# Kernel tuning notes

Measured on AMD Instinct MI355X. Metric: run time of the kernel, lower is better.

Reference implementation:

```python
import jax, jax.numpy as jnp
import numpy as np

H = 128          # hidden_size
EF = 2           # expansion_factor
E = H * EF       # expanded hidden size
K = 4            # conv kernel size
R = 8            # dt_rank = ceil(128/16)
L = 2            # num_layers
BATCH = 2
SEQ = 1024
EPS = 1e-5


def rmsnorm(x, w):
    return x * jax.lax.rsqrt(jnp.mean(x * x, axis=-1, keepdims=True) + EPS) * w


def causal_conv1d(x, w, b):
    # x: (b, l, E); w: (E, 1, K) depthwise; left-pad K-1 => causal, output len l
    xt = jnp.transpose(x, (0, 2, 1))  # (b, E, l)
    out = jax.lax.conv_general_dilated(
        xt, w, window_strides=(1,), padding=[(K - 1, 0)],
        dimension_numbers=("NCH", "OIH", "NCH"), feature_group_count=E)
    out = out + b[None, :, None]
    return jnp.transpose(out, (0, 2, 1))


def sscan(xc, delta, A, Bm, Cm, Dp):
    # xc, delta: (b,l,E); A: (E,n); Bm, Cm: (b,l,n); Dp: (E,)
    deltaA = jnp.exp(jnp.einsum('bld,dn->bldn', delta, A))          # (b,l,E,n)
    deltaBx = jnp.einsum('bld,bln,bld->bldn', delta, Bm, xc)        # (b,l,E,n)

    def step(h, inp):
        dA_t, dBx_t, C_t = inp           # (b,E,n), (b,E,n), (b,n)
        h = dA_t * h + dBx_t
        y = jnp.einsum('bdn,bn->bd', h, C_t)
        return h, y

    b = xc.shape[0]
    h0 = jnp.zeros((b, E, A.shape[1]), dtype=xc.dtype)
    _, ys = jax.lax.scan(
        step, h0,
        (jnp.transpose(deltaA, (1, 0, 2, 3)),
         jnp.transpose(deltaBx, (1, 0, 2, 3)),
         jnp.transpose(Cm, (1, 0, 2))))
    y = jnp.transpose(ys, (1, 0, 2))     # (b,l,E)
    return y + Dp * xc


def mamba_block(x, in_w, in_b, out_w, out_b, pl_w, pl_b, dt_w, dt_b,
                conv_w, conv_b, A_log, Dp):
    xz = x @ in_w + in_b                 # (b,l,2E)
    xc, skip = jnp.split(xz, [E], axis=-1)
    xc = jax.nn.silu(causal_conv1d(xc, conv_w, conv_b))
    # ssm
    A = -jnp.exp(A_log)                  # (E,H)
    dbc = xc @ pl_w + pl_b               # (b,l,R+2H)
    delta, Bm, Cm = jnp.split(dbc, [R, R + H], axis=-1)
    delta = jax.nn.softplus(delta @ dt_w + dt_b)   # (b,l,E)
    y = sscan(xc, delta, A, Bm, Cm, Dp)
    y = y * jax.nn.silu(skip)
    return y @ out_w + out_b


def forward(x, in_w, in_b, out_w, out_b, pl_w, pl_b, dt_w, dt_b,
            conv_w, conv_b, A_log, Dp, norm_w, final_norm_w):
    for i in range(L):
        x = mamba_block(rmsnorm(x, norm_w[i]), in_w[i], in_b[i], out_w[i],
                        out_b[i], pl_w[i], pl_b[i], dt_w[i], dt_b[i],
                        conv_w[i], conv_b[i], A_log[i], Dp[i]) + x
    return rmsnorm(x, final_norm_w)


def setup_inputs() -> dict:
    key = jax.random.key(0)
    ks = jax.random.split(key, 12)
    s = 0.02
    x = jax.random.normal(ks[0], (BATCH, SEQ, H), dtype=jnp.float32)
    in_w = jax.random.normal(ks[1], (L, H, 2 * E)) * s
    in_b = jnp.zeros((L, 2 * E))
    out_w = jax.random.normal(ks[2], (L, E, H)) * s
    out_b = jnp.zeros((L, H))
    pl_w = jax.random.normal(ks[3], (L, E, R + 2 * H)) * s
    pl_b = jnp.zeros((L, R + 2 * H))
    dt_w = jax.random.normal(ks[4], (L, R, E)) * s
    dt_b = jnp.zeros((L, E))
    conv_w = jax.random.normal(ks[5], (L, E, 1, K)) * (1.0 / np.sqrt(K))
    conv_b = jnp.zeros((L, E))
    A_log = jnp.broadcast_to(jnp.log(jnp.arange(1, H + 1, dtype=jnp.float32)),
                             (L, E, H))
    Dp = jnp.ones((L, E))
    norm_w = jnp.ones((L, H))
    final_norm_w = jnp.ones((H,))
    return {"x": x, "in_w": in_w, "in_b": in_b, "out_w": out_w,
            "out_b": out_b, "pl_w": pl_w, "pl_b": pl_b, "dt_w": dt_w,
            "dt_b": dt_b, "conv_w": conv_w, "conv_b": conv_b,
            "A_log": A_log, "Dp": Dp, "norm_w": norm_w,
            "final_norm_w": final_norm_w}


def reference(x, in_w, in_b, out_w, out_b, pl_w, pl_b, dt_w, dt_b,
              conv_w, conv_b, A_log, Dp, norm_w, final_norm_w):
    return forward(x, in_w, in_b, out_w, out_b, pl_w, pl_b, dt_w, dt_b,
                   conv_w, conv_b, A_log, Dp, norm_w, final_norm_w)
```

## Files before the change

kernel.cpp:

```cpp
#include <hip/hip_runtime.h>
#include <hip/hip_bf16.h>

#define HH 128
#define EE 256
#define KK 4
#define RR 8
#define LL 2
#define BB 2
#define SS 1024
#define BT (BB*SS)
#define NJ (RR+2*HH)
#define GG 16
#define CH (SS/GG)
#define EPS 1e-5f
#define LOG2E 1.44269504088896f

__device__ __forceinline__ float silu_f(float v) {
    return v / (1.0f + __expf(-v));
}

__global__ __launch_bounds__(256) void k_wdt(
    const float* __restrict__ plw, const float* __restrict__ plb,
    const float* __restrict__ dtw, const float* __restrict__ dtb,
    float* __restrict__ Wdt, float* __restrict__ bdt)
{
    const int l = blockIdx.x >> 2, q = blockIdx.x & 3;
    const int j = threadIdx.x;
    const float* dtwl = dtw + (size_t)l * RR * EE;
    const float* plwl = plw + (size_t)l * EE * NJ;
    float wr[RR];
    #pragma unroll
    for (int r = 0; r < RR; r++) wr[r] = dtwl[r * EE + j];
    float* Wl = Wdt + (size_t)l * EE * EE;
    for (int e = q * 64; e < q * 64 + 64; e++) {
        float a = 0.0f;
        #pragma unroll
        for (int r = 0; r < RR; r++) a += plwl[(size_t)e * NJ + r] * wr[r];
        Wl[(size_t)e * EE + j] = a;
    }
    if (q == 0) {
        float a = dtb[l * EE + j];
        #pragma unroll
        for (int r = 0; r < RR; r++) a += plb[l * NJ + r] * wr[r];
        bdt[l * EE + j] = a;
    }
}

__global__ __launch_bounds__(512) void k_norm_inproj(
    const float* __restrict__ xin, const float* __restrict__ inw,
    const float* __restrict__ inb, const float* __restrict__ nw,
    float* __restrict__ xz)
{
    __shared__ float xn[8][128];
    const int bt0 = blockIdx.x * 8;
    const int tid = threadIdx.x;
    {
        const int t = tid >> 6, lane = tid & 63;
        const float2 xv = *(const float2*)(xin + (size_t)(bt0 + t) * HH + lane * 2);
        float ss = xv.x*xv.x + xv.y*xv.y;
        #pragma unroll
        for (int m = 32; m >= 1; m >>= 1) ss += __shfl_xor(ss, m);
        const float rs = rsqrtf(ss * (1.0f / HH) + EPS);
        const float2 wv = *(const float2*)(nw + lane * 2);
        xn[t][lane*2+0] = xv.x * rs * wv.x;
        xn[t][lane*2+1] = xv.y * rs * wv.y;
    }
    __syncthreads();
    const int j = tid;
    float acc[8];
    const float bj = inb[j];
    #pragma unroll
    for (int t = 0; t < 8; t++) acc[t] = bj;
    float w0n = inw[0*512 + j], w1n = inw[1*512 + j];
    float w2n = inw[2*512 + j], w3n = inw[3*512 + j];
    for (int k4 = 0; k4 < 32; k4++) {
        const float w0 = w0n, w1 = w1n, w2 = w2n, w3 = w3n;
        if (k4 < 31) {
            const int k = (k4 + 1) * 4;
            w0n = inw[(k+0)*512 + j]; w1n = inw[(k+1)*512 + j];
            w2n = inw[(k+2)*512 + j]; w3n = inw[(k+3)*512 + j];
        }
        const int k = k4 * 4;
        #pragma unroll
        for (int t = 0; t < 8; t++) {
            const float4 xv = *(const float4*)(&xn[t][k]);
            acc[t] += w0*xv.x + w1*xv.y + w2*xv.z + w3*xv.w;
        }
    }
    #pragma unroll
    for (int t = 0; t < 8; t++) xz[(size_t)(bt0 + t) * 512 + j] = acc[t];
}

__global__ __launch_bounds__(512) void k_cbd(
    const float* __restrict__ xz, const float* __restrict__ cw,
    const float* __restrict__ cb, const float* __restrict__ plw,
    const float* __restrict__ plb, const float* __restrict__ Wdt,
    const float* __restrict__ bdt,
    float* __restrict__ xcT, float* __restrict__ BC4,
    float* __restrict__ deltaT, float* __restrict__ sT)
{
    __shared__ float xcb[8][256];
    const int bt0 = blockIdx.x * 8;
    const int tid = threadIdx.x;
    {
        const int e = tid & 255, hf = tid >> 8;
        const int ts = bt0 + hf * 4;
        const float w0 = cw[e*4+0], w1 = cw[e*4+1], w2 = cw[e*4+2], w3 = cw[e*4+3];
        const float bias = cb[e];
        const float* xp = xz + (size_t)ts * 512 + e;
        const bool first = ((ts & (SS-1)) == 0);
        float xm3 = first ? 0.0f : xp[-3*512];
        float xm2 = first ? 0.0f : xp[-2*512];
        float xm1 = first ? 0.0f : xp[-1*512];
        float xcv[4];
        #pragma unroll
        for (int i = 0; i < 4; i++) {
            const float x0 = xp[i*512];
            const float v = bias + w3*x0 + w2*xm1 + w1*xm2 + w0*xm3;
            const float o = silu_f(v);
            xcv[i] = o;
            xcb[hf*4 + i][e] = o;
            xm3 = xm2; xm2 = xm1; xm1 = x0;
        }
        *(float4*)(xcT + (size_t)e * BT + ts) =
            make_float4(xcv[0], xcv[1], xcv[2], xcv[3]);
    }
    __syncthreads();
    const int j = tid & 255, path = tid >> 8;
    if (path == 0) {
        const int nn = j & 127, isC = j >> 7;
        const float* wp = plw + RR + isC * HH + nn;
        float acc[8];
        const float bj = plb[RR + isC * HH + nn];
        #pragma unroll
        for (int t = 0; t < 8; t++) acc[t] = bj;
        float w0n = wp[0*NJ], w1n = wp[1*NJ], w2n = wp[2*NJ], w3n = wp[3*NJ];
        for (int e4 = 0; e4 < 64; e4++) {
            const float w0 = w0n, w1 = w1n, w2 = w2n, w3 = w3n;
            if (e4 < 63) {
                const int e = (e4 + 1) * 4;
                w0n = wp[(size_t)(e+0)*NJ]; w1n = wp[(size_t)(e+1)*NJ];
                w2n = wp[(size_t)(e+2)*NJ]; w3n = wp[(size_t)(e+3)*NJ];
            }
            const int e = e4 * 4;
            #pragma unroll
            for (int t = 0; t < 8; t++) {
                const float4 xv = *(const float4*)(&xcb[t][e]);
                acc[t] += w0*xv.x + w1*xv.y + w2*xv.z + w3*xv.w;
            }
        }
        const int tq0 = bt0 >> 2;
        float* p0 = BC4 + ((size_t)tq0 * 128 + nn) * 8 + isC * 4;
        *(float4*)p0 = make_float4(acc[0], acc[1], acc[2], acc[3]);
        float* p1 = BC4 + ((size_t)(tq0 + 1) * 128 + nn) * 8 + isC * 4;
        *(float4*)p1 = make_float4(acc[4], acc[5], acc[6], acc[7]);
    } else {
        const float* wp = Wdt + j;
        float acc[8];
        const float bj = bdt[j];
        #pragma unroll
        for (int t = 0; t < 8; t++) acc[t] = bj;
        float w0n = wp[0*EE], w1n = wp[1*EE], w2n = wp[2*EE], w3n = wp[3*EE];
        for (int e4 = 0; e4 < 64; e4++) {
            const float w0 = w0n, w1 = w1n, w2 = w2n, w3 = w3n;
            if (e4 < 63) {
                const int e = (e4 + 1) * 4;
                w0n = wp[(size_t)(e+0)*EE]; w1n = wp[(size_t)(e+1)*EE];
                w2n = wp[(size_t)(e+2)*EE]; w3n = wp[(size_t)(e+3)*EE];
            }
            const int e = e4 * 4;
            #pragma unroll
            for (int t = 0; t < 8; t++) {
                const float4 xv = *(const float4*)(&xcb[t][e]);
                acc[t] += w0*xv.x + w1*xv.y + w2*xv.z + w3*xv.w;
            }
        }
        float spv[8], sv[8];
        #pragma unroll
        for (int t = 0; t < 8; t++) {
            const float d = acc[t];
            const float sp = (d > 15.0f) ? d : log1pf(__expf(d));
            spv[t] = sp;
            sv[t] = sp * xcb[t][j];
        }
        float* drp = deltaT + (size_t)j * BT + bt0;
        *(float4*)(drp)     = make_float4(spv[0], spv[1], spv[2], spv[3]);
        *(float4*)(drp + 4) = make_float4(spv[4], spv[5], spv[6], spv[7]);
        float* srp = sT + (size_t)j * BT + bt0;
        *(float4*)(srp)     = make_float4(sv[0], sv[1], sv[2], sv[3]);
        *(float4*)(srp + 4) = make_float4(sv[4], sv[5], sv[6], sv[7]);
    }
}

__global__ __launch_bounds__(128, 4) void k_scan_local(
    const float* __restrict__ BC4, const float* __restrict__ deltaT,
    const float* __restrict__ sT, const float* __restrict__ Alog,
    float* __restrict__ yT, float* __restrict__ hchain,
    float* __restrict__ dsum)
{
    __shared__ float part[2][16][68];
    __shared__ float ybuf[2][CH];
    const int blk = blockIdx.x;
    const int wgid = (blk & 7) * 512 + (blk >> 3);
    const int eq = wgid & 127;
    const int r0 = wgid >> 7;
    const int b = r0 >> 4;
    const int g = r0 & 15;
    const int e0 = eq * 2;
    const int n = threadIdx.x;
    const int t0 = g * CH;

    float An0 = -__expf(Alog[(e0+0) * HH + n]) * LOG2E;
    float An1 = -__expf(Alog[(e0+1) * HH + n]) * LOG2E;
    float h0 = 0.0f, h1 = 0.0f, cum0 = 0.0f, cum1 = 0.0f;
    const float* bc = BC4 + ((size_t)((b * 256 + g * 16) * 128 + n)) * 8;
    const float* dr0 = deltaT + (size_t)(e0+0) * BT + b * SS + t0;
    const float* dr1 = deltaT + (size_t)(e0+1) * BT + b * SS + t0;
    const float* sr0 = sT + (size_t)(e0+0) * BT + b * SS + t0;
    const float* sr1 = sT + (size_t)(e0+1) * BT + b * SS + t0;

    float4 pB = *(const float4*)(bc);
    float4 pC = *(const float4*)(bc + 4);
    float4 pd0 = *(const float4*)dr0, pd1 = *(const float4*)dr1;
    float4 ps0 = *(const float4*)sr0, ps1 = *(const float4*)sr1;

    const int tl = n >> 3, jj = n & 7;
    for (int sc = 0; sc < 4; sc++) {
        #pragma unroll
        for (int q = 0; q < 4; q++) {
            const int qq = sc * 4 + q;
            const float4 cB = pB, cC = pC;
            const float4 cd0 = pd0, cd1 = pd1, cs0 = ps0, cs1 = ps1;
            if (qq < 15) {
                const size_t off = (size_t)(qq + 1) * 1024;
                pB = *(const float4*)(bc + off);
                pC = *(const float4*)(bc + off + 4);
                const int t = (qq + 1) * 4;
                pd0 = *(const float4*)(dr0 + t); pd1 = *(const float4*)(dr1 + t);
                ps0 = *(const float4*)(sr0 + t); ps1 = *(const float4*)(sr1 + t);
            }
            float a;
            a = exp2f(cd0.x*An0); h0 = a*h0 + cs0.x*cB.x; part[0][q*4+0][n] = h0*cC.x;
            a = exp2f(cd0.y*An0); h0 = a*h0 + cs0.y*cB.y; part[0][q*4+1][n] = h0*cC.y;
            a = exp2f(cd0.z*An0); h0 = a*h0 + cs0.z*cB.z; part[0][q*4+2][n] = h0*cC.z;
            a = exp2f(cd0.w*An0); h0 = a*h0 + cs0.w*cB.w; part[0][q*4+3][n] = h0*cC.w;
            a = exp2f(cd1.x*An1); h1 = a*h1 + cs1.x*cB.x; part[1][q*4+0][n] = h1*cC.x;
            a = exp2f(cd1.y*An1); h1 = a*h1 + cs1.y*cB.y; part[1][q*4+1][n] = h1*cC.y;
            a = exp2f(cd1.z*An1); h1 = a*h1 + cs1.z*cB.z; part[1][q*4+2][n] = h1*cC.z;
            a = exp2f(cd1.w*An1); h1 = a*h1 + cs1.w*cB.w; part[1][q*4+3][n] = h1*cC.w;
            cum0 += (cd0.x + cd0.y) + (cd0.z + cd0.w);
            cum1 += (cd1.x + cd1.y) + (cd1.z + cd1.w);
        }
        __syncthreads();
        #pragma unroll
        for (int ee = 0; ee < 2; ee++) {
            float s0 = 0, s1 = 0, s2 = 0, s3 = 0;
            #pragma unroll
            for (int i = 0; i < 4; i++) {
                const float4 p = *(const float4*)(&part[ee][tl][jj*16 + i*4]);
                s0 += p.x; s1 += p.y; s2 += p.z; s3 += p.w;
            }
            float r = (s0 + s1) + (s2 + s3);
            r += __shfl_xor(r, 1); r += __shfl_xor(r, 2); r += __shfl_xor(r, 4);
            if (jj == 0) ybuf[ee][sc*16 + tl] = r;
        }
        __syncthreads();
    }
    {
        const int ee = n >> 6, tt = n & 63;
        yT[(size_t)(e0 + ee) * BT + b * SS + t0 + tt] = ybuf[ee][tt];
    }
    hchain[(size_t)(((b * EE + e0 + 0) * GG) + g) * 128 + n] = h0;
    hchain[(size_t)(((b * EE + e0 + 1) * GG) + g) * 128 + n] = h1;
    if (n == 0) {
        dsum[(b * EE + e0 + 0) * GG + g] = cum0;
        dsum[(b * EE + e0 + 1) * GG + g] = cum1;
    }
}

__global__ __launch_bounds__(128, 4) void k_scan_fix(
    const float* __restrict__ BC4, const float* __restrict__ deltaT,
    const float* __restrict__ Alog, const float* __restrict__ hchain,
    const float* __restrict__ dsum, float* __restrict__ yT)
{
    __shared__ float part[2][16][68];
    __shared__ float ybuf[2][CH];
    const int blk = blockIdx.x;
    const int wgid = (blk & 7) * 480 + (blk >> 3);
    const int eq = wgid & 127;
    const int r0 = wgid >> 7;
    const int b = r0 / 15;
    const int g = 1 + (r0 % 15);
    const int e0 = eq * 2;
    const int n = threadIdx.x;
    const int t0 = g * CH;

    const float An0 = -__expf(Alog[(e0+0) * HH + n]) * LOG2E;
    const float An1 = -__expf(Alog[(e0+1) * HH + n]) * LOG2E;
    float w0 = 0.0f, w1 = 0.0f;
    {
        const size_t hb0 = (size_t)((b * EE + e0 + 0) * GG) * 128 + n;
        const size_t hb1 = (size_t)((b * EE + e0 + 1) * GG) * 128 + n;
        const int db0 = (b * EE + e0 + 0) * GG;
        const int db1 = (b * EE + e0 + 1) * GG;
        for (int gp = 0; gp < g; gp++) {
            const float he0 = hchain[hb0 + (size_t)gp * 128];
            const float he1 = hchain[hb1 + (size_t)gp * 128];
            w0 = exp2f(An0 * dsum[db0 + gp]) * w0 + he0;
            w1 = exp2f(An1 * dsum[db1 + gp]) * w1 + he1;
        }
    }
    float D0 = 0.0f, D1 = 0.0f;
    const float* bc = BC4 + ((size_t)((b * 256 + g * 16) * 128 + n)) * 8;
    const float* dr0 = deltaT + (size_t)(e0+0) * BT + b * SS + t0;
    const float* dr1 = deltaT + (size_t)(e0+1) * BT + b * SS + t0;

    float4 pC = *(const float4*)(bc + 4);
    float4 pd0 = *(const float4*)dr0, pd1 = *(const float4*)dr1;

    const int tl = n >> 3, jj = n & 7;
    for (int sc = 0; sc < 4; sc++) {
        #pragma unroll
        for (int q = 0; q < 4; q++) {
            const int qq = sc * 4 + q;
            const float4 cC = pC;
            const float4 cd0 = pd0, cd1 = pd1;
            if (qq < 15) {
                const size_t off = (size_t)(qq + 1) * 1024;
                pC = *(const float4*)(bc + off + 4);
                const int t = (qq + 1) * 4;
                pd0 = *(const float4*)(dr0 + t); pd1 = *(const float4*)(dr1 + t);
            }
            D0 += cd0.x; part[0][q*4+0][n] = exp2f(An0*D0) * w0 * cC.x;
            D0 += cd0.y; part[0][q*4+1][n] = exp2f(An0*D0) * w0 * cC.y;
            D0 += cd0.z; part[0][q*4+2][n] = exp2f(An0*D0) * w0 * cC.z;
            D0 += cd0.w; part[0][q*4+3][n] = exp2f(An0*D0) * w0 * cC.w;
            D1 += cd1.x; part[1][q*4+0][n] = exp2f(An1*D1) * w1 * cC.x;
            D1 += cd1.y; part[1][q*4+1][n] = exp2f(An1*D1) * w1 * cC.y;
            D1 += cd1.z; part[1][q*4+2][n] = exp2f(An1*D1) * w1 * cC.z;
            D1 += cd1.w; part[1][q*4+3][n] = exp2f(An1*D1) * w1 * cC.w;
        }
        __syncthreads();
        #pragma unroll
        for (int ee = 0; ee < 2; ee++) {
            float s0 = 0, s1 = 0, s2 = 0, s3 = 0;
            #pragma unroll
            for (int i = 0; i < 4; i++) {
                const float4 p = *(const float4*)(&part[ee][tl][jj*16 + i*4]);
                s0 += p.x; s1 += p.y; s2 += p.z; s3 += p.w;
            }
            float r = (s0 + s1) + (s2 + s3);
            r += __shfl_xor(r, 1); r += __shfl_xor(r, 2); r += __shfl_xor(r, 4);
            if (jj == 0) ybuf[ee][sc*16 + tl] = r;
        }
        __syncthreads();
    }
    {
        const int ee = n >> 6, tt = n & 63;
        yT[(size_t)(e0 + ee) * BT + b * SS + t0 + tt] += ybuf[ee][tt];
    }
}

__global__ __launch_bounds__(256) void k_gate(
    const float* __restrict__ yT, const float* __restrict__ xcT,
    const float* __restrict__ xz, const float* __restrict__ Dp,
    const float* __restrict__ ow, const float* __restrict__ ob,
    const float* __restrict__ resin, float* __restrict__ xres)
{
    __shared__ float gs[8][256];
    __shared__ float p2[8][128];
    const int bt0 = blockIdx.x * 8;
    const int tid = threadIdx.x;
    {
        const int e = tid;
        const float dp = Dp[e];
        const float* yp = yT + (size_t)e * BT + bt0;
        const float* xp = xcT + (size_t)e * BT + bt0;
        #pragma unroll
        for (int tq = 0; tq < 2; tq++) {
            const float4 y4 = *(const float4*)(yp + tq * 4);
            const float4 x4 = *(const float4*)(xp + tq * 4);
            float sk;
            sk = xz[(size_t)(bt0 + tq*4 + 0) * 512 + 256 + e];
            gs[tq*4+0][e] = (y4.x + dp * x4.x) * silu_f(sk);
            sk = xz[(size_t)(bt0 + tq*4 + 1) * 512 + 256 + e];
            gs[tq*4+1][e] = (y4.y + dp * x4.y) * silu_f(sk);
            sk = xz[(size_t)(bt0 + tq*4 + 2) * 512 + 256 + e];
            gs[tq*4+2][e] = (y4.z + dp * x4.z) * silu_f(sk);
            sk = xz[(size_t)(bt0 + tq*4 + 3) * 512 + 256 + e];
            gs[tq*4+3][e] = (y4.w + dp * x4.w) * silu_f(sk);
        }
    }
    __syncthreads();
    const int j = tid & 127;
    const int kh = tid >> 7;
    float acc[8];
    #pragma unroll
    for (int t = 0; t < 8; t++) acc[t] = 0.0f;
    const int eb = kh * 128;
    float w0n = ow[(eb+0)*HH + j], w1n = ow[(eb+1)*HH + j];
    float w2n = ow[(eb+2)*HH + j], w3n = ow[(eb+3)*HH + j];
    for (int e4 = 0; e4 < 32; e4++) {
        const float w0 = w0n, w1 = w1n, w2 = w2n, w3 = w3n;
        if (e4 < 31) {
            const int e = eb + (e4 + 1) * 4;
            w0n = ow[(e+0)*HH + j]; w1n = ow[(e+1)*HH + j];
            w2n = ow[(e+2)*HH + j]; w3n = ow[(e+3)*HH + j];
        }
        const int e = eb + e4 * 4;
        #pragma unroll
        for (int t = 0; t < 8; t++) {
            const float4 g4 = *(const float4*)(&gs[t][e]);
            acc[t] += w0*g4.x + w1*g4.y + w2*g4.z + w3*g4.w;
        }
    }
    if (kh == 1) {
        #pragma unroll
        for (int t = 0; t < 8; t++) p2[t][j] = acc[t];
    }
    __syncthreads();
    if (kh == 0) {
        const float bj = ob[j];
        #pragma unroll
        for (int t = 0; t < 8; t++) {
            const float r = acc[t] + p2[t][j] + bj
                          + resin[(size_t)(bt0 + t) * HH + j];
            xres[(size_t)(bt0 + t) * HH + j] = r;
        }
    }
}

__global__ __launch_bounds__(512) void k_finalnorm(
    const float* __restrict__ xres, const float* __restrict__ fw,
    float* __restrict__ out)
{
    const int bt0 = blockIdx.x * 8;
    const int tid = threadIdx.x;
    const int t = tid >> 6, lane = tid & 63;
    const float2 v = *(const float2*)(xres + (size_t)(bt0 + t) * HH + lane * 2);
    float ss = v.x*v.x + v.y*v.y;
    #pragma unroll
    for (int m = 32; m >= 1; m >>= 1) ss += __shfl_xor(ss, m);
    const float rs = rsqrtf(ss * (1.0f / HH) + EPS);
    const float2 w = *(const float2*)(fw + lane * 2);
    float2 o; o.x = v.x * rs * w.x; o.y = v.y * rs * w.y;
    *(float2*)(out + (size_t)(bt0 + t) * HH + lane * 2) = o;
}

extern "C" void kernel_launch(void* const* d_in, const int* in_sizes, int n_in,
                              void* d_out, int out_size, void* d_ws, size_t ws_size,
                              hipStream_t stream)
{
    const float* x      = (const float*)d_in[0];
    const float* in_w   = (const float*)d_in[1];
    const float* in_b   = (const float*)d_in[2];
    const float* out_w  = (const float*)d_in[3];
    const float* out_b  = (const float*)d_in[4];
    const float* pl_w   = (const float*)d_in[5];
    const float* pl_b   = (const float*)d_in[6];
    const float* dt_w   = (const float*)d_in[7];
    const float* dt_b   = (const float*)d_in[8];
    const float* conv_w = (const float*)d_in[9];
    const float* conv_b = (const float*)d_in[10];
    const float* A_log  = (const float*)d_in[11];
    const float* Dp     = (const float*)d_in[12];
    const float* norm_w = (const float*)d_in[13];
    const float* fnw    = (const float*)d_in[14];

    float* ws     = (float*)d_ws;
    float* xres   = ws;
    float* xz     = xres   + 262144;
    float* xcT    = xz     + 1048576;
    float* BC4    = xcT    + 524288;
    float* deltaT = BC4    + 524288;
    float* sT     = deltaT + 524288;
    float* yT     = sT     + 524288;
    float* hchain = yT     + 524288;
    float* dsum   = hchain + 1048576;
    float* Wdt    = dsum   + 8192;
    float* bdt    = Wdt    + 131072;

    k_wdt<<<2*4, 256, 0, stream>>>(pl_w, pl_b, dt_w, dt_b, Wdt, bdt);

    for (int l = 0; l < LL; l++) {
        const float* resin = (l == 0) ? x : xres;
        k_norm_inproj<<<BT/8, 512, 0, stream>>>(
            resin, in_w + (size_t)l*HH*2*EE, in_b + (size_t)l*2*EE,
            norm_w + (size_t)l*HH, xz);
        k_cbd<<<BT/8, 512, 0, stream>>>(
            xz, conv_w + (size_t)l*EE*KK, conv_b + (size_t)l*EE,
            pl_w + (size_t)l*EE*NJ, pl_b + (size_t)l*NJ,
            Wdt + (size_t)l*EE*EE, bdt + (size_t)l*EE,
            xcT, BC4, deltaT, sT);
        k_scan_local<<<BB*GG*(EE/2), 128, 0, stream>>>(
            BC4, deltaT, sT, A_log + (size_t)l*EE*HH, yT, hchain, dsum);
        k_scan_fix<<<BB*(GG-1)*(EE/2), 128, 0, stream>>>(
            BC4, deltaT, A_log + (size_t)l*EE*HH, hchain, dsum, yT);
        k_gate<<<BT/8, 256, 0, stream>>>(
            yT, xcT, xz, Dp + (size_t)l*EE,
            out_w + (size_t)l*EE*HH, out_b + (size_t)l*HH, resin, xres);
    }
    k_finalnorm<<<BT/8, 512, 0, stream>>>(xres, fnw, (float*)d_out);
}
```

Baseline: 231.3 us.

## Fuse norm+inproj with conv kernel, widen scan to 4 channels, fuse final norm

Merges the RMSNorm/in-projection kernel into the conv/projection kernel, recomputing the three halo timesteps of the x half so the conv can read them from shared memory. This avoids the full xz round trip through global memory, and only the z half is stored. The scan kernels now handle 4 channels per block instead of 2, halving block count and sharing B/C loads. The last layer's gate kernel also applies the final norm, removing one launch. The costs are redundant halo matmul work, higher register and LDS pressure, and fewer blocks in flight.

New measurement: 237.3 us. 2.6% more time.

```diff
diff --git a/kernel.cpp b/kernel.cpp
--- a/kernel.cpp
+++ b/kernel.cpp
@@ -46,83 +46,110 @@
     }
 }
 
-__global__ __launch_bounds__(512) void k_norm_inproj(
-    const float* __restrict__ xin, const float* __restrict__ inw,
+__global__ __launch_bounds__(512) void k_front(
+    const float* __restrict__ resin, const float* __restrict__ inw,
     const float* __restrict__ inb, const float* __restrict__ nw,
-    float* __restrict__ xz)
+    const float* __restrict__ cw, const float* __restrict__ cb,
+    const float* __restrict__ plw, const float* __restrict__ plb,
+    const float* __restrict__ Wdt, const float* __restrict__ bdt,
+    float* __restrict__ zbuf, float* __restrict__ xcT,
+    float* __restrict__ BC4, float* __restrict__ deltaT,
+    float* __restrict__ sT)
 {
-    __shared__ float xn[8][128];
-    const int bt0 = blockIdx.x * 8;
-    const int tid = threadIdx.x;
-    {
-        const int t = tid >> 6, lane = tid & 63;
-        const float2 xv = *(const float2*)(xin + (size_t)(bt0 + t) * HH + lane * 2);
-        float ss = xv.x*xv.x + xv.y*xv.y;
-        #pragma unroll
-        for (int m = 32; m >= 1; m >>= 1) ss += __shfl_xor(ss, m);
-        const float rs = rsqrtf(ss * (1.0f / HH) + EPS);
-        const float2 wv = *(const float2*)(nw + lane * 2);
-        xn[t][lane*2+0] = xv.x * rs * wv.x;
-        xn[t][lane*2+1] = xv.y * rs * wv.y;
-    }
-    __syncthreads();
-    const int j = tid;
-    float acc[8];
-    const float bj = inb[j];
-    #pragma unroll
-    for (int t = 0; t < 8; t++) acc[t] = bj;
-    float w0n = inw[0*512 + j], w1n = inw[1*512 + j];
-    float w2n = inw[2*512 + j], w3n = inw[3*512 + j];
-    for (int k4 = 0; k4 < 32; k4++) {
-        const float w0 = w0n, w1 = w1n, w2 = w2n, w3 = w3n;
-        if (k4 < 31) {
-            const int k = (k4 + 1) * 4;
-            w0n = inw[(k+0)*512 + j]; w1n = inw[(k+1)*512 + j];
-            w2n = inw[(k+2)*512 + j]; w3n = inw[(k+3)*512 + j];
-        }
-        const int k = k4 * 4;
-        #pragma unroll
-        for (int t = 0; t < 8; t++) {
-            const float4 xv = *(const float4*)(&xn[t][k]);
-            acc[t] += w0*xv.x + w1*xv.y + w2*xv.z + w3*xv.w;
-        }
-    }
-    #pragma unroll
-    for (int t = 0; t < 8; t++) xz[(size_t)(bt0 + t) * 512 + j] = acc[t];
-}
-
-__global__ __launch_bounds__(512) void k_cbd(
-    const float* __restrict__ xz, const float* __restrict__ cw,
-    const float* __restrict__ cb, const float* __restrict__ plw,
-    const float* __restrict__ plb, const float* __restrict__ Wdt,
-    const float* __restrict__ bdt,
-    float* __restrict__ xcT, float* __restrict__ BC4,
-    float* __restrict__ deltaT, float* __restrict__ sT)
-{
+    __shared__ float xn[11][132];
+    __shared__ float xci[11][256];
     __shared__ float xcb[8][256];
     const int bt0 = blockIdx.x * 8;
     const int tid = threadIdx.x;
+    const int lb = ((bt0 & (SS - 1)) == 0) ? 0 : 3;
+    {
+        const int tt = tid >> 5, lane = tid & 31;
+        if (tt < lb + 8) {
+            const int bt = bt0 - lb + tt;
+            const float4 xv = *(const float4*)(resin + (size_t)bt * HH + lane * 4);
+            float ss = xv.x*xv.x + xv.y*xv.y + xv.z*xv.z + xv.w*xv.w;
+            ss += __shfl_xor(ss, 16); ss += __shfl_xor(ss, 8);
+            ss += __shfl_xor(ss, 4);  ss += __shfl_xor(ss, 2);
+            ss += __shfl_xor(ss, 1);
+            const float rs = rsqrtf(ss * (1.0f / HH) + EPS);
+            const float4 wv = *(const float4*)(nw + lane * 4);
+            xn[tt][lane*4+0] = xv.x * rs * wv.x;
+            xn[tt][lane*4+1] = xv.y * rs * wv.y;
+            xn[tt][lane*4+2] = xv.z * rs * wv.z;
+            xn[tt][lane*4+3] = xv.w * rs * wv.w;
+        }
+    }
+    __syncthreads();
+    if (tid < 256) {
+        const int j = tid;
+        float acc[11];
+        const float bj = inb[j];
+        #pragma unroll
+        for (int t = 0; t < 11; t++) acc[t] = bj;
+        float w0n = inw[0*512 + j], w1n = inw[1*512 + j];
+        float w2n = inw[2*512 + j], w3n = inw[3*512 + j];
+        for (int k4 = 0; k4 < 32; k4++) {
+            const float w0 = w0n, w1 = w1n, w2 = w2n, w3 = w3n;
+            if (k4 < 31) {
+                const int k = (k4 + 1) * 4;
+                w0n = inw[(k+0)*512 + j]; w1n = inw[(k+1)*512 + j];
+                w2n = inw[(k+2)*512 + j]; w3n = inw[(k+3)*512 + j];
+            }
+            const int k = k4 * 4;
+            #pragma unroll
+            for (int t = 0; t < 11; t++) {
+                const float4 xv = *(const float4*)(&xn[t][k]);
+                acc[t] += w0*xv.x + w1*xv.y + w2*xv.z + w3*xv.w;
+            }
+        }
+        #pragma unroll
+        for (int t = 0; t < 11; t++)
+            if (t < lb + 8) xci[t][j] = acc[t];
+    } else {
+        const int j = tid - 256;
+        float acc[8];
+        const float bj = inb[256 + j];
+        #pragma unroll
+        for (int t = 0; t < 8; t++) acc[t] = bj;
+        float w0n = inw[0*512 + 256 + j], w1n = inw[1*512 + 256 + j];
+        float w2n = inw[2*512 + 256 + j], w3n = inw[3*512 + 256 + j];
+        for (int k4 = 0; k4 < 32; k4++) {
+            const float w0 = w0n, w1 = w1n, w2 = w2n, w3 = w3n;
+            if (k4 < 31) {
+                const int k = (k4 + 1) * 4;
+                w0n = inw[(k+0)*512 + 256 + j]; w1n = inw[(k+1)*512 + 256 + j];
+                w2n = inw[(k+2)*512 + 256 + j]; w3n = inw[(k+3)*512 + 256 + j];
+            }
+            const int k = k4 * 4;
+            #pragma unroll
+            for (int t = 0; t < 8; t++) {
+                const float4 xv = *(const float4*)(&xn[lb + t][k]);
+                acc[t] += w0*xv.x + w1*xv.y + w2*xv.z + w3*xv.w;
+            }
+        }
+        #pragma unroll
+        for (int t = 0; t < 8; t++)
+            zbuf[(size_t)(bt0 + t) * 256 + j] = acc[t];
+    }
+    __syncthreads();
     {
         const int e = tid & 255, hf = tid >> 8;
-        const int ts = bt0 + hf * 4;
         const float w0 = cw[e*4+0], w1 = cw[e*4+1], w2 = cw[e*4+2], w3 = cw[e*4+3];
         const float bias = cb[e];
-        const float* xp = xz + (size_t)ts * 512 + e;
-        const bool first = ((ts & (SS-1)) == 0);
-        float xm3 = first ? 0.0f : xp[-3*512];
-        float xm2 = first ? 0.0f : xp[-2*512];
-        float xm1 = first ? 0.0f : xp[-1*512];
         float xcv[4];
         #pragma unroll
         for (int i = 0; i < 4; i++) {
-            const float x0 = xp[i*512];
-            const float v = bias + w3*x0 + w2*xm1 + w1*xm2 + w0*xm3;
+            const int m = lb + hf * 4 + i;
+            const float a0  = xci[m][e];
+            const float am1 = (m >= 1) ? xci[m-1][e] : 0.0f;
+            const float am2 = (m >= 2) ? xci[m-2][e] : 0.0f;
+            const float am3 = (m >= 3) ? xci[m-3][e] : 0.0f;
+            const float v = bias + w3*a0 + w2*am1 + w1*am2 + w0*am3;
             const float o = silu_f(v);
             xcv[i] = o;
             xcb[hf*4 + i][e] = o;
-            xm3 = xm2; xm2 = xm1; xm1 = x0;
-        }
-        *(float4*)(xcT + (size_t)e * BT + ts) =
+        }
+        *(float4*)(xcT + (size_t)e * BT + bt0 + hf * 4) =
             make_float4(xcv[0], xcv[1], xcv[2], xcv[3]);
     }
     __syncthreads();
@@ -198,62 +225,76 @@
     float* __restrict__ yT, float* __restrict__ hchain,
     float* __restrict__ dsum)
 {
-    __shared__ float part[2][16][68];
-    __shared__ float ybuf[2][CH];
+    __shared__ float part[4][16][68];
+    __shared__ float ybuf[4][CH];
     const int blk = blockIdx.x;
-    const int wgid = (blk & 7) * 512 + (blk >> 3);
-    const int eq = wgid & 127;
-    const int r0 = wgid >> 7;
+    const int wgid = (blk & 7) * 256 + (blk >> 3);
+    const int eq = wgid & 63;
+    const int r0 = wgid >> 6;
     const int b = r0 >> 4;
     const int g = r0 & 15;
-    const int e0 = eq * 2;
+    const int e0 = eq * 4;
     const int n = threadIdx.x;
     const int t0 = g * CH;
 
-    float An0 = -__expf(Alog[(e0+0) * HH + n]) * LOG2E;
-    float An1 = -__expf(Alog[(e0+1) * HH + n]) * LOG2E;
-    float h0 = 0.0f, h1 = 0.0f, cum0 = 0.0f, cum1 = 0.0f;
+    float An[4], h[4], cum[4];
+    #pragma unroll
+    for (int ee = 0; ee < 4; ee++) {
+        An[ee] = -__expf(Alog[(e0 + ee) * HH + n]) * LOG2E;
+        h[ee] = 0.0f; cum[ee] = 0.0f;
+    }
     const float* bc = BC4 + ((size_t)((b * 256 + g * 16) * 128 + n)) * 8;
-    const float* dr0 = deltaT + (size_t)(e0+0) * BT + b * SS + t0;
-    const float* dr1 = deltaT + (size_t)(e0+1) * BT + b * SS + t0;
-    const float* sr0 = sT + (size_t)(e0+0) * BT + b * SS + t0;
-    const float* sr1 = sT + (size_t)(e0+1) * BT + b * SS + t0;
-
+    const float* dr[4]; const float* sr[4];
+    #pragma unroll
+    for (int ee = 0; ee < 4; ee++) {
+        dr[ee] = deltaT + (size_t)(e0 + ee) * BT + b * SS + t0;
+        sr[ee] = sT + (size_t)(e0 + ee) * BT + b * SS + t0;
+    }
     float4 pB = *(const float4*)(bc);
     float4 pC = *(const float4*)(bc + 4);
-    float4 pd0 = *(const float4*)dr0, pd1 = *(const float4*)dr1;
-    float4 ps0 = *(const float4*)sr0, ps1 = *(const float4*)sr1;
-
+    float4 pd[4], ps[4];
+    #pragma unroll
+    for (int ee = 0; ee < 4; ee++) {
+        pd[ee] = *(const float4*)dr[ee];
+        ps[ee] = *(const float4*)sr[ee];
+    }
     const int tl = n >> 3, jj = n & 7;
     for (int sc = 0; sc < 4; sc++) {
         #pragma unroll
         for (int q = 0; q < 4; q++) {
             const int qq = sc * 4 + q;
             const float4 cB = pB, cC = pC;
-            const float4 cd0 = pd0, cd1 = pd1, cs0 = ps0, cs1 = ps1;
+            float4 cd[4], cs[4];
+            #pragma unroll
+            for (int ee = 0; ee < 4; ee++) { cd[ee] = pd[ee]; cs[ee] = ps[ee]; }
             if (qq < 15) {
                 const size_t off = (size_t)(qq + 1) * 1024;
                 pB = *(const float4*)(bc + off);
                 pC = *(const float4*)(bc + off + 4);
                 const int t = (qq + 1) * 4;
-                pd0 = *(const float4*)(dr0 + t); pd1 = *(const float4*)(dr1 + t);
-                ps0 = *(const float4*)(sr0 + t); ps1 = *(const float4*)(sr1 + t);
-            }
-            float a;
-            a = exp2f(cd0.x*An0); h0 = a*h0 + cs0.x*cB.x; part[0][q*4+0][n] = h0*cC.x;
-            a = exp2f(cd0.y*An0); h0 = a*h0 + cs0.y*cB.y; part[0][q*4+1][n] = h0*cC.y;
-            a = exp2f(cd0.z*An0); h0 = a*h0 + cs0.z*cB.z; part[0][q*4+2][n] = h0*cC.z;
-            a = exp2f(cd0.w*An0); h0 = a*h0 + cs0.w*cB.w; part[0][q*4+3][n] = h0*cC.w;
-            a = exp2f(cd1.x*An1); h1 = a*h1 + cs1.x*cB.x; part[1][q*4+0][n] = h1*cC.x;
-            a = exp2f(cd1.y*An1); h1 = a*h1 + cs1.y*cB.y; part[1][q*4+1][n] = h1*cC.y;
-            a = exp2f(cd1.z*An1); h1 = a*h1 + cs1.z*cB.z; part[1][q*4+2][n] = h1*cC.z;
-            a = exp2f(cd1.w*An1); h1 = a*h1 + cs1.w*cB.w; part[1][q*4+3][n] = h1*cC.w;
-            cum0 += (cd0.x + cd0.y) + (cd0.z + cd0.w);
-            cum1 += (cd1.x + cd1.y) + (cd1.z + cd1.w);
+                #pragma unroll
+                for (int ee = 0; ee < 4; ee++) {
+                    pd[ee] = *(const float4*)(dr[ee] + t);
+                    ps[ee] = *(const float4*)(sr[ee] + t);
+                }
+            }
+            #pragma unroll
+            for (int ee = 0; ee < 4; ee++) {
+                float a;
+                a = exp2f(cd[ee].x*An[ee]); h[ee] = a*h[ee] + cs[ee].x*cB.x;
+                part[ee][q*4+0][n] = h[ee]*cC.x;
+                a = exp2f(cd[ee].y*An[ee]); h[ee] = a*h[ee] + cs[ee].y*cB.y;
+                part[ee][q*4+1][n] = h[ee]*cC.y;
+                a = exp2f(cd[ee].z*An[ee]); h[ee] = a*h[ee] + cs[ee].z*cB.z;
+                part[ee][q*4+2][n] = h[ee]*cC.z;
+                a = exp2f(cd[ee].w*An[ee]); h[ee] = a*h[ee] + cs[ee].w*cB.w;
+                part[ee][q*4+3][n] = h[ee]*cC.w;
+                cum[ee] += (cd[ee].x + cd[ee].y) + (cd[ee].z + cd[ee].w);
+            }
         }
         __syncthreads();
         #pragma unroll
-        for (int ee = 0; ee < 2; ee++) {
+        for (int ee = 0; ee < 4; ee++) {
             float s0 = 0, s1 = 0, s2 = 0, s3 = 0;
             #pragma unroll
             for (int i = 0; i < 4; i++) {
@@ -267,14 +308,18 @@
         __syncthreads();
     }
     {
-        const int ee = n >> 6, tt = n & 63;
-        yT[(size_t)(e0 + ee) * BT + b * SS + t0 + tt] = ybuf[ee][tt];
-    }
-    hchain[(size_t)(((b * EE + e0 + 0) * GG) + g) * 128 + n] = h0;
-    hchain[(size_t)(((b * EE + e0 + 1) * GG) + g) * 128 + n] = h1;
+        const int ee = n >> 5, tt = n & 31;
+        float* yp = yT + (size_t)(e0 + ee) * BT + b * SS + t0;
+        yp[tt] = ybuf[ee][tt];
+        yp[tt + 32] = ybuf[ee][tt + 32];
+    }
+    #pragma unroll
+    for (int ee = 0; ee < 4; ee++)
+        hchain[(size_t)(((b * EE + e0 + ee) * GG) + g) * 128 + n] = h[ee];
     if (n == 0) {
-        dsum[(b * EE + e0 + 0) * GG + g] = cum0;
-        dsum[(b * EE + e0 + 1) * GG + g] = cum1;
+        #pragma unroll
+        for (int ee = 0; ee < 4; ee++)
+            dsum[(b * EE + e0 + ee) * GG + g] = cum[ee];
     }
 }
 
@@ -283,40 +328,44 @@
     const float* __restrict__ Alog, const float* __restrict__ hchain,
     const float* __restrict__ dsum, float* __restrict__ yT)
 {
-    __shared__ float part[2][16][68];
-    __shared__ float ybuf[2][CH];
+    __shared__ float part[4][16][68];
+    __shared__ float ybuf[4][CH];
     const int blk = blockIdx.x;
-    const int wgid = (blk & 7) * 480 + (blk >> 3);
-    const int eq = wgid & 127;
-    const int r0 = wgid >> 7;
+    const int wgid = (blk & 7) * 240 + (blk >> 3);
+    const int eq = wgid & 63;
+    const int r0 = wgid >> 6;
     const int b = r0 / 15;
     const int g = 1 + (r0 % 15);
-    const int e0 = eq * 2;
+    const int e0 = eq * 4;
     const int n = threadIdx.x;
     const int t0 = g * CH;
 
-    const float An0 = -__expf(Alog[(e0+0) * HH + n]) * LOG2E;
-    const float An1 = -__expf(Alog[(e0+1) * HH + n]) * LOG2E;
-    float w0 = 0.0f, w1 = 0.0f;
-    {
-        const size_t hb0 = (size_t)((b * EE + e0 + 0) * GG) * 128 + n;
-        const size_t hb1 = (size_t)((b * EE + e0 + 1) * GG) * 128 + n;
-        const int db0 = (b * EE + e0 + 0) * GG;
-        const int db1 = (b * EE + e0 + 1) * GG;
+    float An[4], w[4], D[4];
+    #pragma unroll
+    for (int ee = 0; ee < 4; ee++) {
+        An[ee] = -__expf(Alog[(e0 + ee) * HH + n]) * LOG2E;
+        w[ee] = 0.0f; D[ee] = 0.0f;
+    }
+    {
         for (int gp = 0; gp < g; gp++) {
-            const float he0 = hchain[hb0 + (size_t)gp * 128];
-            const float he1 = hchain[hb1 + (size_t)gp * 128];
-            w0 = exp2f(An0 * dsum[db0 + gp]) * w0 + he0;
-            w1 = exp2f(An1 * dsum[db1 + gp]) * w1 + he1;
-        }
-    }
-    float D0 = 0.0f, D1 = 0.0f;
+            #pragma unroll
+            for (int ee = 0; ee < 4; ee++) {
+                const float he = hchain[(size_t)(((b * EE + e0 + ee) * GG) + gp) * 128 + n];
+                const float ds = dsum[(b * EE + e0 + ee) * GG + gp];
+                w[ee] = exp2f(An[ee] * ds) * w[ee] + he;
+            }
+        }
+    }
     const float* bc = BC4 + ((size_t)((b * 256 + g * 16) * 128 + n)) * 8;
-    const float* dr0 = deltaT + (size_t)(e0+0) * BT + b * SS + t0;
-    const float* dr1 = deltaT + (size_t)(e0+1) * BT + b * SS + t0;
+    const float* dr[4];
+    #pragma unroll
+    for (int ee = 0; ee < 4; ee++)
+        dr[ee] = deltaT + (size_t)(e0 + ee) * BT + b * SS + t0;
 
     float4 pC = *(const float4*)(bc + 4);
-    float4 pd0 = *(const float4*)dr0, pd1 = *(const float4*)dr1;
+    float4 pd[4];
+    #pragma unroll
+    for (int ee = 0; ee < 4; ee++) pd[ee] = *(const float4*)dr[ee];
 
     const int tl = n >> 3, jj = n & 7;
     for (int sc = 0; sc < 4; sc++) {
@@ -324,25 +373,28 @@
         for (int q = 0; q < 4; q++) {
             const int qq = sc * 4 + q;
             const float4 cC = pC;
-            const float4 cd0 = pd0, cd1 = pd1;
+            float4 cd[4];
+            #pragma unroll
+            for (int ee = 0; ee < 4; ee++) cd[ee] = pd[ee];
             if (qq < 15) {
                 const size_t off = (size_t)(qq + 1) * 1024;
                 pC = *(const float4*)(bc + off + 4);
                 const int t = (qq + 1) * 4;
-                pd0 = *(const float4*)(dr0 + t); pd1 = *(const float4*)(dr1 + t);
-            }
-            D0 += cd0.x; part[0][q*4+0][n] = exp2f(An0*D0) * w0 * cC.x;
-            D0 += cd0.y; part[0][q*4+1][n] = exp2f(An0*D0) * w0 * cC.y;
-            D0 += cd0.z; part[0][q*4+2][n] = exp2f(An0*D0) * w0 * cC.z;
-            D0 += cd0.w; part[0][q*4+3][n] = exp2f(An0*D0) * w0 * cC.w;
-            D1 += cd1.x; part[1][q*4+0][n] = exp2f(An1*D1) * w1 * cC.x;
-            D1 += cd1.y; part[1][q*4+1][n] = exp2f(An1*D1) * w1 * cC.y;
-            D1 += cd1.z; part[1][q*4+2][n] = exp2f(An1*D1) * w1 * cC.z;
-            D1 += cd1.w; part[1][q*4+3][n] = exp2f(An1*D1) * w1 * cC.w;
+                #pragma unroll
+                for (int ee = 0; ee < 4; ee++)
+                    pd[ee] = *(const float4*)(dr[ee] + t);
+            }
+            #pragma unroll
+            for (int ee = 0; ee < 4; ee++) {
+                D[ee] += cd[ee].x; part[ee][q*4+0][n] = exp2f(An[ee]*D[ee]) * w[ee] * cC.x;
+                D[ee] += cd[ee].y; part[ee][q*4+1][n] = exp2f(An[ee]*D[ee]) * w[ee] * cC.y;
+                D[ee] += cd[ee].z; part[ee][q*4+2][n] = exp2f(An[ee]*D[ee]) * w[ee] * cC.z;
+                D[ee] += cd[ee].w; part[ee][q*4+3][n] = exp2f(An[ee]*D[ee]) * w[ee] * cC.w;
+            }
         }
         __syncthreads();
         #pragma unroll
-        for (int ee = 0; ee < 2; ee++) {
+        for (int ee = 0; ee < 4; ee++) {
             float s0 = 0, s1 = 0, s2 = 0, s3 = 0;
             #pragma unroll
             for (int i = 0; i < 4; i++) {
@@ -356,14 +408,16 @@
         __syncthreads();
     }
     {
-        const int ee = n >> 6, tt = n & 63;
-        yT[(size_t)(e0 + ee) * BT + b * SS + t0 + tt] += ybuf[ee][tt];
+        const int ee = n >> 5, tt = n & 31;
+        float* yp = yT + (size_t)(e0 + ee) * BT + b * SS + t0;
+        yp[tt] += ybuf[ee][tt];
+        yp[tt + 32] += ybuf[ee][tt + 32];
     }
 }
 
 __global__ __launch_bounds__(256) void k_gate(
     const float* __restrict__ yT, const float* __restrict__ xcT,
-    const float* __restrict__ xz, const float* __restrict__ Dp,
+    const float* __restrict__ zbuf, const float* __restrict__ Dp,
     const float* __restrict__ ow, const float* __restrict__ ob,
     const float* __restrict__ resin, float* __restrict__ xres)
 {
@@ -381,13 +435,13 @@
             const float4 y4 = *(const float4*)(yp + tq * 4);
             const float4 x4 = *(const float4*)(xp + tq * 4);
             float sk;
-            sk = xz[(size_t)(bt0 + tq*4 + 0) * 512 + 256 + e];
+            sk = zbuf[(size_t)(bt0 + tq*4 + 0) * 256 + e];
             gs[tq*4+0][e] = (y4.x + dp * x4.x) * silu_f(sk);
-            sk = xz[(size_t)(bt0 + tq*4 + 1) * 512 + 256 + e];
+            sk = zbuf[(size_t)(bt0 + tq*4 + 1) * 256 + e];
             gs[tq*4+1][e] = (y4.y + dp * x4.y) * silu_f(sk);
-            sk = xz[(size_t)(bt0 + tq*4 + 2) * 512 + 256 + e];
+            sk = zbuf[(size_t)(bt0 + tq*4 + 2) * 256 + e];
             gs[tq*4+2][e] = (y4.z + dp * x4.z) * silu_f(sk);
-            sk = xz[(size_t)(bt0 + tq*4 + 3) * 512 + 256 + e];
+            sk = zbuf[(size_t)(bt0 + tq*4 + 3) * 256 + e];
             gs[tq*4+3][e] = (y4.w + dp * x4.w) * silu_f(sk);
         }
     }
@@ -430,21 +484,91 @@
     }
 }
 
-__global__ __launch_bounds__(512) void k_finalnorm(
-    const float* __restrict__ xres, const float* __restrict__ fw,
+__global__ __launch_bounds__(256) void k_gate_final(
+    const float* __restrict__ yT, const float* __restrict__ xcT,
+    const float* __restrict__ zbuf, const float* __restrict__ Dp,
+    const float* __restrict__ ow, const float* __restrict__ ob,
+    const float* __restrict__ resin, const float* __restrict__ fw,
     float* __restrict__ out)
 {
+    __shared__ float gs[8][256];
+    __shared__ float p2[8][132];
     const int bt0 = blockIdx.x * 8;
     const int tid = threadIdx.x;
-    const int t = tid >> 6, lane = tid & 63;
-    const float2 v = *(const float2*)(xres + (size_t)(bt0 + t) * HH + lane * 2);
-    float ss = v.x*v.x + v.y*v.y;
-    #pragma unroll
-    for (int m = 32; m >= 1; m >>= 1) ss += __shfl_xor(ss, m);
-    const float rs = rsqrtf(ss * (1.0f / HH) + EPS);
-    const float2 w = *(const float2*)(fw + lane * 2);
-    float2 o; o.x = v.x * rs * w.x; o.y = v.y * rs * w.y;
-    *(float2*)(out + (size_t)(bt0 + t) * HH + lane * 2) = o;
+    {
+        const int e = tid;
+        const float dp = Dp[e];
+        const float* yp = yT + (size_t)e * BT + bt0;
+        const float* xp = xcT + (size_t)e * BT + bt0;
+        #pragma unroll
+        for (int tq = 0; tq < 2; tq++) {
+            const float4 y4 = *(const float4*)(yp + tq * 4);
+            const float4 x4 = *(const float4*)(xp + tq * 4);
+            float sk;
+            sk = zbuf[(size_t)(bt0 + tq*4 + 0) * 256 + e];
+            gs[tq*4+0][e] = (y4.x + dp * x4.x) * silu_f(sk);
+            sk = zbuf[(size_t)(bt0 + tq*4 + 1) * 256 + e];
+            gs[tq*4+1][e] = (y4.y + dp * x4.y) * silu_f(sk);
+            sk = zbuf[(size_t)(bt0 + tq*4 + 2) * 256 + e];
+            gs[tq*4+2][e] = (y4.z + dp * x4.z) * silu_f(sk);
+            sk = zbuf[(size_t)(bt0 + tq*4 + 3) * 256 + e];
+            gs[tq*4+3][e] = (y4.w + dp * x4.w) * silu_f(sk);
+        }
+    }
+    __syncthreads();
+    const int j = tid & 127;
+    const int kh = tid >> 7;
+    {
+        float acc[8];
+        #pragma unroll
+        for (int t = 0; t < 8; t++) acc[t] = 0.0f;
+        const int eb = kh * 128;
+        float w0n = ow[(eb+0)*HH + j], w1n = ow[(eb+1)*HH + j];
+        float w2n = ow[(eb+2)*HH + j], w3n = ow[(eb+3)*HH + j];
+        for (int e4 = 0; e4 < 32; e4++) {
+            const float w0 = w0n, w1 = w1n, w2 = w2n, w3 = w3n;
+            if (e4 < 31) {
+                const int e = eb + (e4 + 1) * 4;
+                w0n = ow[(e+0)*HH + j]; w1n = ow[(e+1)*HH + j];
+                w2n = ow[(e+2)*HH + j]; w3n = ow[(e+3)*HH + j];
+            }
+            const int e = eb + e4 * 4;
+            #pragma unroll
+            for (int t = 0; t < 8; t++) {
+                const float4 g4 = *(const float4*)(&gs[t][e]);
+                acc[t] += w0*g4.x + w1*g4.y + w2*g4.z + w3*g4.w;
+            }
+        }
+        if (kh == 1) {
+            #pragma unroll
+            for (int t = 0; t < 8; t++) p2[t][j] = acc[t];
+        }
+        __syncthreads();
+        if (kh == 0) {
+            const float bj = ob[j];
+            #pragma unroll
+            for (int t = 0; t < 8; t++) {
+                const float r = acc[t] + p2[t][j] + bj
+                              + resin[(size_t)(bt0 + t) * HH + j];
+                p2[t][j] = r;
+            }
+        }
+    }
+    __syncthreads();
+    {
+        const int t = tid >> 5, lane = tid & 31;
+        const float4 v = *(const float4*)(&p2[t][lane * 4]);
+        float ss = v.x*v.x + v.y*v.y + v.z*v.z + v.w*v.w;
+        ss += __shfl_xor(ss, 16); ss += __shfl_xor(ss, 8);
+        ss += __shfl_xor(ss, 4);  ss += __shfl_xor(ss, 2);
+        ss += __shfl_xor(ss, 1);
+        const float rs = rsqrtf(ss * (1.0f / HH) + EPS);
+        const float4 w = *(const float4*)(fw + lane * 4);
+        float4 o;
+        o.x = v.x * rs * w.x; o.y = v.y * rs * w.y;
+        o.z = v.z * rs * w.z; o.w = v.w * rs * w.w;
+        *(float4*)(out + (size_t)(bt0 + t) * HH + lane * 4) = o;
+    }
 }
 
 extern "C" void kernel_launch(void* const* d_in, const int* in_sizes, int n_in,
@@ -469,8 +593,8 @@
 
     float* ws     = (float*)d_ws;
     float* xres   = ws;
-    float* xz     = xres   + 262144;
-    float* xcT    = xz     + 1048576;
+    float* zbuf   = xres   + 262144;
+    float* xcT    = zbuf   + 524288;
     float* BC4    = xcT    + 524288;
     float* deltaT = BC4    + 524288;
     float* sT     = deltaT + 524288;
@@ -484,21 +608,26 @@
 
     for (int l = 0; l < LL; l++) {
         const float* resin = (l == 0) ? x : xres;
-        k_norm_inproj<<<BT/8, 512, 0, stream>>>(
+        k_front<<<BT/8, 512, 0, stream>>>(
             resin, in_w + (size_t)l*HH*2*EE, in_b + (size_t)l*2*EE,
-            norm_w + (size_t)l*HH, xz);
-        k_cbd<<<BT/8, 512, 0, stream>>>(
-            xz, conv_w + (size_t)l*EE*KK, conv_b + (size_t)l*EE,
+            norm_w + (size_t)l*HH,
+            conv_w + (size_t)l*EE*KK, conv_b + (size_t)l*EE,
             pl_w + (size_t)l*EE*NJ, pl_b + (size_t)l*NJ,
             Wdt + (size_t)l*EE*EE, bdt + (size_t)l*EE,
-            xcT, BC4, deltaT, sT);
-        k_scan_local<<<BB*GG*(EE/2), 128, 0, stream>>>(
+            zbuf, xcT, BC4, deltaT, sT);
+        k_scan_local<<<BB*GG*(EE/4), 128, 0, stream>>>(
             BC4, deltaT, sT, A_log + (size_t)l*EE*HH, yT, hchain, dsum);
-        k_scan_fix<<<BB*(GG-1)*(EE/2), 128, 0, stream>>>(
+        k_scan_fix<<<BB*(GG-1)*(EE/4), 128, 0, stream>>>(
             BC4, deltaT, A_log + (size_t)l*EE*HH, hchain, dsum, yT);
-        k_gate<<<BT/8, 256, 0, stream>>>(
-            yT, xcT, xz, Dp + (size_t)l*EE,
-            out_w + (size_t)l*EE*HH, out_b + (size_t)l*HH, resin, xres);
-    }
-    k_finalnorm<<<BT/8, 512, 0, stream>>>(xres, fnw, (float*)d_out);
-}
+        if (l < LL - 1) {
+            k_gate<<<BT/8, 256, 0, stream>>>(
+                yT, xcT, zbuf, Dp + (size_t)l*EE,
+                out_w + (size_t)l*EE*HH, out_b + (size_t)l*HH, resin, xres);
+        } else {
+            k_gate_final<<<BT/8, 256, 0, stream>>>(
+                yT, xcT, zbuf, Dp + (size_t)l*EE,
+                out_w + (size_t)l*EE*HH, out_b + (size_t)l*HH, xres,
+                fnw, (float*)d_out);
+        }
+    }
+}
```
